# Kernel optimization log

Hardware: AMD Instinct MI355X
Metric: run time of the kernel (lower is better)

The kernel has to match this reference:

```python
import jax, jax.numpy as jnp
import numpy as np

N, D, HID, ATT, B, NC = 131072, 1024, 256, 128, 64, 2
EPS = 1e-5

def _ln(h, g, b):
    mu = jnp.mean(h, axis=-1, keepdims=True)
    var = jnp.mean((h - mu) ** 2, axis=-1, keepdims=True)
    return (h - mu) * jax.lax.rsqrt(var + EPS) * g + b

def _gelu(x):
    return jax.nn.gelu(x, approximate=False)  # torch nn.GELU default (erf)

def setup_inputs() -> dict:
    key = jax.random.key(0)
    ks = jax.random.split(key, 16)
    def w(k, shape, fan_in):
        return (jax.random.normal(k, shape, jnp.float32) / np.sqrt(fan_in)).astype(jnp.float32)
    # sorted, every bag non-empty (~equal sizes)
    segment_ids = ((jnp.arange(N) * B) // N).astype(jnp.int32)
    return {
        "x": jax.random.normal(ks[0], (N, D), jnp.float32),
        "segment_ids": segment_ids,
        "W1": w(ks[1], (D, HID), D), "b1": jnp.zeros((HID,), jnp.float32),
        "g1": jnp.ones((HID,), jnp.float32), "be1": jnp.zeros((HID,), jnp.float32),
        "W2": w(ks[2], (HID, HID), HID), "b2": jnp.zeros((HID,), jnp.float32),
        "g2": jnp.ones((HID,), jnp.float32), "be2": jnp.zeros((HID,), jnp.float32),
        "Wv": w(ks[3], (HID, ATT), HID), "bv": jnp.zeros((ATT,), jnp.float32),
        "Wu": w(ks[4], (HID, ATT), HID), "bu": jnp.zeros((ATT,), jnp.float32),
        "Ww": w(ks[5], (ATT, 1), ATT), "bw": jnp.zeros((1,), jnp.float32),
        "Wc1": w(ks[6], (HID, HID // 2), HID), "bc1": jnp.zeros((HID // 2,), jnp.float32),
        "Wc2": w(ks[7], (HID // 2, NC), HID // 2), "bc2": jnp.zeros((NC,), jnp.float32),
    }

def reference(x, segment_ids, W1, b1, g1, be1, W2, b2, g2, be2,
              Wv, bv, Wu, bu, Ww, bw, Wc1, bc1, Wc2, bc2):
    # encoder (dropout = identity at inference)
    h = _gelu(_ln(x @ W1 + b1, g1, be1))          # [N, HID]
    h = _gelu(_ln(h @ W2 + b2, g2, be2))          # [N, HID]
    # gated attention logits
    a = (jnp.tanh(h @ Wv + bv) * jax.nn.sigmoid(h @ Wu + bu)) @ Ww + bw  # [N, 1]
    a = a[:, 0]                                    # [N]
    # per-bag (segment) softmax
    m = jax.ops.segment_max(a, segment_ids, num_segments=B)             # [B]
    e = jnp.exp(a - m[segment_ids])
    s = jax.ops.segment_sum(e, segment_ids, num_segments=B)             # [B]
    attn = e / s[segment_ids]                                           # [N]
    # attention-weighted bag pooling
    z = jax.ops.segment_sum(attn[:, None] * h, segment_ids, num_segments=B)  # [B, HID]
    # classifier
    logits = _gelu(z @ Wc1 + bc1) @ Wc2 + bc2       # [B, NC]
    return logits
```

## Files before the change

kernel.cpp:

```cpp
#include <hip/hip_runtime.h>
#include <math.h>

#define N_TOK  131072
#define DIM    1024
#define HIDN   256
#define ATTN   128
#define NSEG   64
#define SEGLEN 2048
#define NCLS   2
#define EPSLN  1e-5f

typedef __attribute__((ext_vector_type(8))) short  short8;
typedef __attribute__((ext_vector_type(4))) float  f32x4;

__device__ __forceinline__ unsigned short f2bf(float f) {
    unsigned int u = __float_as_uint(f);
    u += 0x7fffu + ((u >> 16) & 1u);
    return (unsigned short)(u >> 16);
}
__device__ __forceinline__ float bf2f(unsigned short h) {
    return __uint_as_float(((unsigned int)h) << 16);
}
__device__ __forceinline__ float gelu_exact(float x) {
    return 0.5f * x * (1.0f + erff(x * 0.70710678118654752f));
}

__global__ __launch_bounds__(256) void transpose_cvt(const float* __restrict__ in,
                                                     unsigned short* __restrict__ out,
                                                     int R, int C) {
    __shared__ float t[32][33];
    const int bx = blockIdx.x * 32;
    const int by = blockIdx.y * 32;
    const int x = threadIdx.x, y = threadIdx.y;
#pragma unroll
    for (int i = 0; i < 32; i += 8) {
        int r = by + y + i, c = bx + x;
        if (r < R && c < C) t[y + i][x] = in[(size_t)r * C + c];
    }
    __syncthreads();
#pragma unroll
    for (int i = 0; i < 32; i += 8) {
        int c = bx + y + i, r = by + x;
        if (c < C && r < R) out[(size_t)c * R + r] = f2bf(t[x][y + i]);
    }
}

__global__ void build_bvu(const float* __restrict__ bv, const float* __restrict__ bu,
                          float* __restrict__ bvu) {
    int t = threadIdx.x;
    bvu[t] = (t < 128) ? bv[t] : bu[t - 128];
}

template <int K, int MODE, bool AF32>
__global__ __launch_bounds__(256, 3) void gemm_fused(const void* __restrict__ Aptr,
                                                     const unsigned short* __restrict__ Wt,
                                                     const float* __restrict__ bias,
                                                     const float* __restrict__ g,
                                                     const float* __restrict__ be,
                                                     unsigned short* __restrict__ Hout,
                                                     const float* __restrict__ Ww,
                                                     const float* __restrict__ bw,
                                                     float* __restrict__ Aout) {
    constexpr int NT = K / 32;
    __shared__ __align__(16) char smem[51200];
    auto As0 = (unsigned short (*)[40])(smem);
    auto As1 = (unsigned short (*)[40])(smem + 5120);
    auto Ws0 = (unsigned short (*)[40])(smem + 10240);
    auto Ws1 = (unsigned short (*)[40])(smem + 10240 + 20480);

    const int tid  = threadIdx.x;
    const int wave = tid >> 6, lane = tid & 63;
    const int lr = lane & 15, lq = lane >> 4;
    const int srow = tid >> 2, skq = (tid & 3) * 8;
    const size_t row0 = (size_t)blockIdx.x * 64;

    f32x4 acc[4][4];
#pragma unroll
    for (int i = 0; i < 4; i++)
#pragma unroll
        for (int j = 0; j < 4; j++) acc[i][j] = (f32x4)0.0f;

    auto loadA = [&](int k0, short8& aw) {
        if constexpr (AF32) {
            const float* A = (const float*)Aptr;
            const float* p = &A[(row0 + srow) * K + k0 + skq];
            float4 v0 = *(const float4*)p;
            float4 v1 = *(const float4*)(p + 4);
            aw[0] = (short)f2bf(v0.x); aw[1] = (short)f2bf(v0.y);
            aw[2] = (short)f2bf(v0.z); aw[3] = (short)f2bf(v0.w);
            aw[4] = (short)f2bf(v1.x); aw[5] = (short)f2bf(v1.y);
            aw[6] = (short)f2bf(v1.z); aw[7] = (short)f2bf(v1.w);
        } else {
            const unsigned short* A = (const unsigned short*)Aptr;
            aw = *(const short8*)&A[(row0 + srow) * K + k0 + skq];
        }
    };
    auto loadW = [&](int k0, short8* ww) {
#pragma unroll
        for (int c = 0; c < 4; c++)
            ww[c] = *(const short8*)&Wt[(size_t)(srow + 64 * c) * K + k0 + skq];
    };
    auto writeT = [&](unsigned short (*As)[40], unsigned short (*Ws)[40],
                      const short8& aw, const short8* ww) {
        *(short8*)&As[srow][skq] = aw;
#pragma unroll
        for (int c = 0; c < 4; c++)
            *(short8*)&Ws[srow + 64 * c][skq] = ww[c];
    };
    auto mmaT = [&](unsigned short (*As)[40], unsigned short (*Ws)[40]) {
        short8 a[4], b[4];
#pragma unroll
        for (int i = 0; i < 4; i++) a[i] = *(const short8*)&As[16 * i + lr][lq * 8];
#pragma unroll
        for (int j = 0; j < 4; j++) b[j] = *(const short8*)&Ws[64 * wave + 16 * j + lr][lq * 8];
#pragma unroll
        for (int i = 0; i < 4; i++)
#pragma unroll
            for (int j = 0; j < 4; j++)
                acc[i][j] = __builtin_amdgcn_mfma_f32_16x16x32_bf16(a[i], b[j], acc[i][j], 0, 0, 0);
    };

    short8 aw;
    short8 ww[4];
    loadA(0, aw);
    loadW(0, ww);
    writeT(As0, Ws0, aw, ww);
    __syncthreads();

    for (int t = 0; t < NT; t += 2) {
        loadA(32 * (t + 1), aw);
        loadW(32 * (t + 1), ww);
        mmaT(As0, Ws0);
        writeT(As1, Ws1, aw, ww);
        __syncthreads();
        if (t + 2 < NT) {
            loadA(32 * (t + 2), aw);
            loadW(32 * (t + 2), ww);
        }
        mmaT(As1, Ws1);
        if (t + 2 < NT) writeT(As0, Ws0, aw, ww);
        __syncthreads();
    }

    float bjv[4];
#pragma unroll
    for (int j = 0; j < 4; j++) bjv[j] = bias[wave * 64 + 16 * j + lr];
#pragma unroll
    for (int i = 0; i < 4; i++)
#pragma unroll
        for (int j = 0; j < 4; j++)
#pragma unroll
            for (int r = 0; r < 4; r++) acc[i][j][r] += bjv[j];

    if constexpr (MODE == 0) {
        float (*red)[4][64] = (float (*)[4][64])smem;
#pragma unroll
        for (int i = 0; i < 4; i++)
#pragma unroll
            for (int r = 0; r < 4; r++) {
                float s = 0.0f, sq = 0.0f;
#pragma unroll
                for (int j = 0; j < 4; j++) { float v = acc[i][j][r]; s += v; sq += v * v; }
#pragma unroll
                for (int m = 1; m < 16; m <<= 1) { s += __shfl_xor(s, m); sq += __shfl_xor(sq, m); }
                if (lr == 0) {
                    red[0][wave][16 * i + 4 * lq + r] = s;
                    red[1][wave][16 * i + 4 * lq + r] = sq;
                }
            }
        __syncthreads();
        float gj[4], bej[4];
#pragma unroll
        for (int j = 0; j < 4; j++) {
            gj[j]  = g[wave * 64 + 16 * j + lr];
            bej[j] = be[wave * 64 + 16 * j + lr];
        }
#pragma unroll
        for (int i = 0; i < 4; i++)
#pragma unroll
            for (int r = 0; r < 4; r++) {
                const int row = 16 * i + 4 * lq + r;
                const float s  = red[0][0][row] + red[0][1][row] + red[0][2][row] + red[0][3][row];
                const float sq = red[1][0][row] + red[1][1][row] + red[1][2][row] + red[1][3][row];
                const float mu  = s * (1.0f / HIDN);
                const float var = sq * (1.0f / HIDN) - mu * mu;
                const float rs  = rsqrtf(var + EPSLN);
#pragma unroll
                for (int j = 0; j < 4; j++) {
                    const float o = (acc[i][j][r] - mu) * rs * gj[j] + bej[j];
                    Hout[(row0 + row) * 256 + wave * 64 + 16 * j + lr] = f2bf(gelu_exact(o));
                }
            }
    } else {
        float (*us)[129] = (float (*)[129])smem;
        float (*pw)[64]  = (float (*)[64])(smem + 33024);
        if (wave >= 2) {
            const int cb = (wave - 2) * 64;
#pragma unroll
            for (int i = 0; i < 4; i++)
#pragma unroll
                for (int j = 0; j < 4; j++)
#pragma unroll
                    for (int r = 0; r < 4; r++)
                        us[16 * i + 4 * lq + r][cb + 16 * j + lr] =
                            1.0f / (1.0f + expf(-acc[i][j][r]));
        }
        __syncthreads();
        if (wave < 2) {
            const int cb = wave * 64;
            float wwj[4];
#pragma unroll
            for (int j = 0; j < 4; j++) wwj[j] = Ww[cb + 16 * j + lr];
#pragma unroll
            for (int i = 0; i < 4; i++)
#pragma unroll
                for (int r = 0; r < 4; r++) {
                    const int row = 16 * i + 4 * lq + r;
                    float s = 0.0f;
#pragma unroll
                    for (int j = 0; j < 4; j++)
                        s += tanhf(acc[i][j][r]) * us[row][cb + 16 * j + lr] * wwj[j];
#pragma unroll
                    for (int m = 1; m < 16; m <<= 1) s += __shfl_xor(s, m);
                    if (lr == 0) pw[wave][row] = s;
                }
        }
        __syncthreads();
        if (tid < 64) Aout[row0 + tid] = pw[0][tid] + pw[1][tid] + bw[0];
    }
}

__global__ __launch_bounds__(256) void seg_softmax(float* __restrict__ A) {
    __shared__ float red[256];
    const int seg = blockIdx.x, tid = threadIdx.x;
    float* a = A + (size_t)seg * SEGLEN;
    float m = -1e30f;
#pragma unroll
    for (int c = 0; c < 8; c++) m = fmaxf(m, a[tid + 256 * c]);
    red[tid] = m; __syncthreads();
    for (int s = 128; s > 0; s >>= 1) {
        if (tid < s) red[tid] = fmaxf(red[tid], red[tid + s]);
        __syncthreads();
    }
    m = red[0]; __syncthreads();
    float e[8]; float sum = 0.0f;
#pragma unroll
    for (int c = 0; c < 8; c++) { e[c] = expf(a[tid + 256 * c] - m); sum += e[c]; }
    red[tid] = sum; __syncthreads();
    for (int s = 128; s > 0; s >>= 1) {
        if (tid < s) red[tid] += red[tid + s];
        __syncthreads();
    }
    const float inv = 1.0f / red[0];
#pragma unroll
    for (int c = 0; c < 8; c++) a[tid + 256 * c] = e[c] * inv;
}

__global__ __launch_bounds__(256) void pool_partial(const float* __restrict__ Attn,
                                                    const unsigned short* __restrict__ H,
                                                    float* __restrict__ Zp) {
    __shared__ float aw[256];
    __shared__ float part[8][256];
    const int tid = threadIdx.x;
    const size_t rbase = (size_t)blockIdx.x * 256;
    aw[tid] = Attn[rbase + tid];
    __syncthreads();
    const int cg = tid & 31;
    const int rg = tid >> 5;
    float acc[8];
#pragma unroll
    for (int j = 0; j < 8; j++) acc[j] = 0.0f;
    for (int r = rg * 32; r < rg * 32 + 32; ++r) {
        short8 h8 = *(const short8*)&H[(rbase + r) * 256 + cg * 8];
        const float a = aw[r];
#pragma unroll
        for (int j = 0; j < 8; j++) acc[j] += a * bf2f((unsigned short)h8[j]);
    }
#pragma unroll
    for (int j = 0; j < 8; j++) part[rg][cg * 8 + j] = acc[j];
    __syncthreads();
    float s = 0.0f;
#pragma unroll
    for (int gq = 0; gq < 8; gq++) s += part[gq][tid];
    Zp[rbase + tid] = s;
}

__global__ __launch_bounds__(256) void head_kernel(const float* __restrict__ Zp,
                                                   const float* __restrict__ Wc1,
                                                   const float* __restrict__ bc1,
                                                   const float* __restrict__ Wc2,
                                                   const float* __restrict__ bc2,
                                                   float* __restrict__ Out) {
    __shared__ float zs[256];
    __shared__ float hs[128];
    __shared__ float red[4];
    const int seg = blockIdx.x, tid = threadIdx.x;
    float z = 0.0f;
#pragma unroll
    for (int c = 0; c < 8; c++) z += Zp[((size_t)seg * 8 + c) * 256 + tid];
    zs[tid] = z;
    __syncthreads();
    if (tid < 128) {
        float acc = bc1[tid];
        for (int k = 0; k < 256; k++) acc += zs[k] * Wc1[k * 128 + tid];
        hs[tid] = gelu_exact(acc);
    }
    __syncthreads();
    const int cls = tid >> 7, j = tid & 127;
    float val = hs[j] * Wc2[j * 2 + cls];
#pragma unroll
    for (int o = 32; o > 0; o >>= 1) val += __shfl_down(val, o);
    if ((tid & 63) == 0) red[tid >> 6] = val;
    __syncthreads();
    if (tid < 2) Out[seg * 2 + tid] = red[tid * 2] + red[tid * 2 + 1] + bc2[tid];
}

extern "C" void kernel_launch(void* const* d_in, const int* in_sizes, int n_in,
                              void* d_out, int out_size, void* d_ws, size_t ws_size,
                              hipStream_t stream) {
    const float* x   = (const float*)d_in[0];
    const float* W1  = (const float*)d_in[2];
    const float* b1  = (const float*)d_in[3];
    const float* g1  = (const float*)d_in[4];
    const float* be1 = (const float*)d_in[5];
    const float* W2  = (const float*)d_in[6];
    const float* b2  = (const float*)d_in[7];
    const float* g2  = (const float*)d_in[8];
    const float* be2 = (const float*)d_in[9];
    const float* Wv  = (const float*)d_in[10];
    const float* bv  = (const float*)d_in[11];
    const float* Wu  = (const float*)d_in[12];
    const float* bu  = (const float*)d_in[13];
    const float* Ww  = (const float*)d_in[14];
    const float* bw  = (const float*)d_in[15];
    const float* Wc1 = (const float*)d_in[16];
    const float* bc1 = (const float*)d_in[17];
    const float* Wc2 = (const float*)d_in[18];
    const float* bc2 = (const float*)d_in[19];
    float* out = (float*)d_out;

    char* p = (char*)d_ws;
    unsigned short* h1b    = (unsigned short*)p; p += (size_t)N_TOK * HIDN * 2;
    unsigned short* h2b    = (unsigned short*)p; p += (size_t)N_TOK * HIDN * 2;
    float*          scores = (float*)p;          p += (size_t)N_TOK * 4;
    unsigned short* W1t    = (unsigned short*)p; p += (size_t)HIDN * DIM * 2;
    unsigned short* W2t    = (unsigned short*)p; p += (size_t)HIDN * HIDN * 2;
    unsigned short* Wvut   = (unsigned short*)p; p += (size_t)HIDN * HIDN * 2;
    float*          bvu    = (float*)p;          p += 256 * 4;
    float*          Zp     = (float*)p;          p += (size_t)NSEG * 8 * HIDN * 4;

    dim3 tb(32, 8);
    transpose_cvt<<<dim3(HIDN / 32, DIM / 32), tb, 0, stream>>>(W1, W1t, DIM, HIDN);
    transpose_cvt<<<dim3(HIDN / 32, HIDN / 32), tb, 0, stream>>>(W2, W2t, HIDN, HIDN);
    transpose_cvt<<<dim3(ATTN / 32, HIDN / 32), tb, 0, stream>>>(Wv, Wvut, HIDN, ATTN);
    transpose_cvt<<<dim3(ATTN / 32, HIDN / 32), tb, 0, stream>>>(Wu, Wvut + (size_t)ATTN * HIDN, HIDN, ATTN);
    build_bvu<<<1, 256, 0, stream>>>(bv, bu, bvu);

    gemm_fused<DIM, 0, true><<<N_TOK / 64, 256, 0, stream>>>(
        x, W1t, b1, g1, be1, h1b, nullptr, nullptr, nullptr);
    gemm_fused<HIDN, 0, false><<<N_TOK / 64, 256, 0, stream>>>(
        h1b, W2t, b2, g2, be2, h2b, nullptr, nullptr, nullptr);
    gemm_fused<HIDN, 1, false><<<N_TOK / 64, 256, 0, stream>>>(
        h2b, Wvut, bvu, nullptr, nullptr, nullptr, Ww, bw, scores);

    seg_softmax<<<NSEG, 256, 0, stream>>>(scores);
    pool_partial<<<NSEG * 8, 256, 0, stream>>>(scores, h2b, Zp);
    head_kernel<<<NSEG, 256, 0, stream>>>(Zp, Wc1, bc1, Wc2, bc2, out);
}
```

Measured before the change: 1.007 ms.

## Fuse encoder MLP and attention scoring into one kernel, drop softmax pass

Merges the three per-token GEMM kernels into one kernel that keeps the first hidden layer in LDS, so the h1 round trip to global memory and the re-read of h2 for scoring are gone. Weights for the second and third GEMMs are read straight from global memory. The separate softmax kernel is removed: pool_partial exponentiates the raw scores and also writes per-block exp sums, and the head kernel divides by the segment total. The four transpose kernels and the bias-packing kernel become one launch. In exchange, the first GEMM loses its double-buffered LDS pipeline, and skipping the max subtraction relies on the gated scores staying bounded enough that exp does not overflow.

```diff
diff --git a/kernel.cpp b/kernel.cpp
--- a/kernel.cpp
+++ b/kernel.cpp
@@ -25,48 +25,51 @@
     return 0.5f * x * (1.0f + erff(x * 0.70710678118654752f));
 }
 
-__global__ __launch_bounds__(256) void transpose_cvt(const float* __restrict__ in,
-                                                     unsigned short* __restrict__ out,
-                                                     int R, int C) {
+__global__ __launch_bounds__(256) void prep_weights(const float* __restrict__ W1,
+                                                    const float* __restrict__ W2,
+                                                    const float* __restrict__ Wv,
+                                                    const float* __restrict__ Wu,
+                                                    const float* __restrict__ bv,
+                                                    const float* __restrict__ bu,
+                                                    unsigned short* __restrict__ W1t,
+                                                    unsigned short* __restrict__ W2t,
+                                                    unsigned short* __restrict__ Wvut,
+                                                    float* __restrict__ bvu) {
+    const int b = blockIdx.x;
+    const int x = threadIdx.x, y = threadIdx.y;
+    if (b == 384) {
+        const int t = y * 32 + x;
+        bvu[t] = (t < 128) ? bv[t] : bu[t - 128];
+        return;
+    }
+    const float* in; unsigned short* out; int R, C, tx, ty;
+    if (b < 256)      { in = W1; out = W1t;                        R = DIM;  C = HIDN; tx = b & 7;         ty = b >> 3; }
+    else if (b < 320) { in = W2; out = W2t;                        R = HIDN; C = HIDN; tx = (b - 256) & 7; ty = (b - 256) >> 3; }
+    else if (b < 352) { in = Wv; out = Wvut;                       R = HIDN; C = ATTN; tx = (b - 320) & 3; ty = (b - 320) >> 2; }
+    else              { in = Wu; out = Wvut + (size_t)ATTN * HIDN; R = HIDN; C = ATTN; tx = (b - 352) & 3; ty = (b - 352) >> 2; }
     __shared__ float t[32][33];
-    const int bx = blockIdx.x * 32;
-    const int by = blockIdx.y * 32;
-    const int x = threadIdx.x, y = threadIdx.y;
-#pragma unroll
-    for (int i = 0; i < 32; i += 8) {
-        int r = by + y + i, c = bx + x;
-        if (r < R && c < C) t[y + i][x] = in[(size_t)r * C + c];
-    }
-    __syncthreads();
-#pragma unroll
-    for (int i = 0; i < 32; i += 8) {
-        int c = bx + y + i, r = by + x;
-        if (c < C && r < R) out[(size_t)c * R + r] = f2bf(t[x][y + i]);
-    }
-}
-
-__global__ void build_bvu(const float* __restrict__ bv, const float* __restrict__ bu,
-                          float* __restrict__ bvu) {
-    int t = threadIdx.x;
-    bvu[t] = (t < 128) ? bv[t] : bu[t - 128];
-}
-
-template <int K, int MODE, bool AF32>
-__global__ __launch_bounds__(256, 3) void gemm_fused(const void* __restrict__ Aptr,
-                                                     const unsigned short* __restrict__ Wt,
-                                                     const float* __restrict__ bias,
-                                                     const float* __restrict__ g,
-                                                     const float* __restrict__ be,
-                                                     unsigned short* __restrict__ Hout,
-                                                     const float* __restrict__ Ww,
-                                                     const float* __restrict__ bw,
-                                                     float* __restrict__ Aout) {
-    constexpr int NT = K / 32;
-    __shared__ __align__(16) char smem[51200];
-    auto As0 = (unsigned short (*)[40])(smem);
-    auto As1 = (unsigned short (*)[40])(smem + 5120);
-    auto Ws0 = (unsigned short (*)[40])(smem + 10240);
-    auto Ws1 = (unsigned short (*)[40])(smem + 10240 + 20480);
+    const int bx = tx * 32, by = ty * 32;
+#pragma unroll
+    for (int i = 0; i < 32; i += 8) t[y + i][x] = in[(size_t)(by + y + i) * C + bx + x];
+    __syncthreads();
+#pragma unroll
+    for (int i = 0; i < 32; i += 8) out[(size_t)(bx + y + i) * R + by + x] = f2bf(t[x][y + i]);
+}
+
+__global__ __launch_bounds__(256, 3) void fused_mlp_score(
+    const float* __restrict__ x,
+    const unsigned short* __restrict__ W1t,
+    const unsigned short* __restrict__ W2t,
+    const unsigned short* __restrict__ Wvut,
+    const float* __restrict__ b1, const float* __restrict__ g1, const float* __restrict__ be1,
+    const float* __restrict__ b2, const float* __restrict__ g2, const float* __restrict__ be2,
+    const float* __restrict__ bvu, const float* __restrict__ Ww, const float* __restrict__ bw,
+    unsigned short* __restrict__ h2b, float* __restrict__ scores) {
+    __shared__ __align__(16) char smem[35840];
+    auto As  = (unsigned short (*)[40])smem;
+    auto Ws  = (unsigned short (*)[40])(smem + 5120);
+    auto HT  = (unsigned short (*)[264])smem;
+    auto red = (float (*)[4][64])(smem + 33792);
 
     const int tid  = threadIdx.x;
     const int wave = tid >> 6, lane = tid & 63;
@@ -75,85 +78,23 @@
     const size_t row0 = (size_t)blockIdx.x * 64;
 
     f32x4 acc[4][4];
-#pragma unroll
-    for (int i = 0; i < 4; i++)
-#pragma unroll
-        for (int j = 0; j < 4; j++) acc[i][j] = (f32x4)0.0f;
-
-    auto loadA = [&](int k0, short8& aw) {
-        if constexpr (AF32) {
-            const float* A = (const float*)Aptr;
-            const float* p = &A[(row0 + srow) * K + k0 + skq];
-            float4 v0 = *(const float4*)p;
-            float4 v1 = *(const float4*)(p + 4);
-            aw[0] = (short)f2bf(v0.x); aw[1] = (short)f2bf(v0.y);
-            aw[2] = (short)f2bf(v0.z); aw[3] = (short)f2bf(v0.w);
-            aw[4] = (short)f2bf(v1.x); aw[5] = (short)f2bf(v1.y);
-            aw[6] = (short)f2bf(v1.z); aw[7] = (short)f2bf(v1.w);
-        } else {
-            const unsigned short* A = (const unsigned short*)Aptr;
-            aw = *(const short8*)&A[(row0 + srow) * K + k0 + skq];
-        }
+    auto zero_acc = [&]() {
+#pragma unroll
+        for (int i = 0; i < 4; i++)
+#pragma unroll
+            for (int j = 0; j < 4; j++) acc[i][j] = (f32x4)0.0f;
     };
-    auto loadW = [&](int k0, short8* ww) {
-#pragma unroll
-        for (int c = 0; c < 4; c++)
-            ww[c] = *(const short8*)&Wt[(size_t)(srow + 64 * c) * K + k0 + skq];
-    };
-    auto writeT = [&](unsigned short (*As)[40], unsigned short (*Ws)[40],
-                      const short8& aw, const short8* ww) {
-        *(short8*)&As[srow][skq] = aw;
-#pragma unroll
-        for (int c = 0; c < 4; c++)
-            *(short8*)&Ws[srow + 64 * c][skq] = ww[c];
-    };
-    auto mmaT = [&](unsigned short (*As)[40], unsigned short (*Ws)[40]) {
-        short8 a[4], b[4];
-#pragma unroll
-        for (int i = 0; i < 4; i++) a[i] = *(const short8*)&As[16 * i + lr][lq * 8];
-#pragma unroll
-        for (int j = 0; j < 4; j++) b[j] = *(const short8*)&Ws[64 * wave + 16 * j + lr][lq * 8];
-#pragma unroll
-        for (int i = 0; i < 4; i++)
-#pragma unroll
-            for (int j = 0; j < 4; j++)
-                acc[i][j] = __builtin_amdgcn_mfma_f32_16x16x32_bf16(a[i], b[j], acc[i][j], 0, 0, 0);
-    };
-
-    short8 aw;
-    short8 ww[4];
-    loadA(0, aw);
-    loadW(0, ww);
-    writeT(As0, Ws0, aw, ww);
-    __syncthreads();
-
-    for (int t = 0; t < NT; t += 2) {
-        loadA(32 * (t + 1), aw);
-        loadW(32 * (t + 1), ww);
-        mmaT(As0, Ws0);
-        writeT(As1, Ws1, aw, ww);
-        __syncthreads();
-        if (t + 2 < NT) {
-            loadA(32 * (t + 2), aw);
-            loadW(32 * (t + 2), ww);
-        }
-        mmaT(As1, Ws1);
-        if (t + 2 < NT) writeT(As0, Ws0, aw, ww);
-        __syncthreads();
-    }
-
-    float bjv[4];
-#pragma unroll
-    for (int j = 0; j < 4; j++) bjv[j] = bias[wave * 64 + 16 * j + lr];
-#pragma unroll
-    for (int i = 0; i < 4; i++)
-#pragma unroll
-        for (int j = 0; j < 4; j++)
-#pragma unroll
-            for (int r = 0; r < 4; r++) acc[i][j][r] += bjv[j];
-
-    if constexpr (MODE == 0) {
-        float (*red)[4][64] = (float (*)[4][64])smem;
+
+    auto ln_epilogue = [&](const float* bias, const float* gamma, const float* beta, bool toGlobal) {
+        float bjv[4];
+#pragma unroll
+        for (int j = 0; j < 4; j++) bjv[j] = bias[wave * 64 + 16 * j + lr];
+#pragma unroll
+        for (int i = 0; i < 4; i++)
+#pragma unroll
+            for (int j = 0; j < 4; j++)
+#pragma unroll
+                for (int r = 0; r < 4; r++) acc[i][j][r] += bjv[j];
 #pragma unroll
         for (int i = 0; i < 4; i++)
 #pragma unroll
@@ -172,8 +113,8 @@
         float gj[4], bej[4];
 #pragma unroll
         for (int j = 0; j < 4; j++) {
-            gj[j]  = g[wave * 64 + 16 * j + lr];
-            bej[j] = be[wave * 64 + 16 * j + lr];
+            gj[j]  = gamma[wave * 64 + 16 * j + lr];
+            bej[j] = beta[wave * 64 + 16 * j + lr];
         }
 #pragma unroll
         for (int i = 0; i < 4; i++)
@@ -187,13 +128,99 @@
                 const float rs  = rsqrtf(var + EPSLN);
 #pragma unroll
                 for (int j = 0; j < 4; j++) {
-                    const float o = (acc[i][j][r] - mu) * rs * gj[j] + bej[j];
-                    Hout[(row0 + row) * 256 + wave * 64 + 16 * j + lr] = f2bf(gelu_exact(o));
+                    const int col = wave * 64 + 16 * j + lr;
+                    const unsigned short hv = f2bf(gelu_exact((acc[i][j][r] - mu) * rs * gj[j] + bej[j]));
+                    HT[row][col] = hv;
+                    if (toGlobal) h2b[(row0 + row) * 256 + col] = hv;
                 }
             }
-    } else {
+        __syncthreads();
+    };
+
+    zero_acc();
+    for (int k0 = 0; k0 < DIM; k0 += 32) {
+        const float* p = &x[(row0 + srow) * DIM + k0 + skq];
+        float4 v0 = *(const float4*)p;
+        float4 v1 = *(const float4*)(p + 4);
+        short8 aw;
+        aw[0] = (short)f2bf(v0.x); aw[1] = (short)f2bf(v0.y);
+        aw[2] = (short)f2bf(v0.z); aw[3] = (short)f2bf(v0.w);
+        aw[4] = (short)f2bf(v1.x); aw[5] = (short)f2bf(v1.y);
+        aw[6] = (short)f2bf(v1.z); aw[7] = (short)f2bf(v1.w);
+        short8 ww[4];
+#pragma unroll
+        for (int c = 0; c < 4; c++)
+            ww[c] = *(const short8*)&W1t[(size_t)(srow + 64 * c) * DIM + k0 + skq];
+        __syncthreads();
+        *(short8*)&As[srow][skq] = aw;
+#pragma unroll
+        for (int c = 0; c < 4; c++)
+            *(short8*)&Ws[srow + 64 * c][skq] = ww[c];
+        __syncthreads();
+        short8 a[4], b[4];
+#pragma unroll
+        for (int i = 0; i < 4; i++) a[i] = *(const short8*)&As[16 * i + lr][lq * 8];
+#pragma unroll
+        for (int j = 0; j < 4; j++) b[j] = *(const short8*)&Ws[64 * wave + 16 * j + lr][lq * 8];
+#pragma unroll
+        for (int i = 0; i < 4; i++)
+#pragma unroll
+            for (int j = 0; j < 4; j++)
+                acc[i][j] = __builtin_amdgcn_mfma_f32_16x16x32_bf16(a[i], b[j], acc[i][j], 0, 0, 0);
+    }
+    __syncthreads();
+    ln_epilogue(b1, g1, be1, false);
+
+    zero_acc();
+#pragma unroll 2
+    for (int t = 0; t < 8; t++) {
+        const int k0 = t * 32;
+        short8 a[4], b[4];
+#pragma unroll
+        for (int j = 0; j < 4; j++)
+            b[j] = *(const short8*)&W2t[(size_t)(64 * wave + 16 * j + lr) * HIDN + k0 + lq * 8];
+#pragma unroll
+        for (int i = 0; i < 4; i++) a[i] = *(const short8*)&HT[16 * i + lr][k0 + lq * 8];
+#pragma unroll
+        for (int i = 0; i < 4; i++)
+#pragma unroll
+            for (int j = 0; j < 4; j++)
+                acc[i][j] = __builtin_amdgcn_mfma_f32_16x16x32_bf16(a[i], b[j], acc[i][j], 0, 0, 0);
+    }
+    __syncthreads();
+    ln_epilogue(b2, g2, be2, true);
+
+    zero_acc();
+#pragma unroll 2
+    for (int t = 0; t < 8; t++) {
+        const int k0 = t * 32;
+        short8 a[4], b[4];
+#pragma unroll
+        for (int j = 0; j < 4; j++)
+            b[j] = *(const short8*)&Wvut[(size_t)(64 * wave + 16 * j + lr) * HIDN + k0 + lq * 8];
+#pragma unroll
+        for (int i = 0; i < 4; i++) a[i] = *(const short8*)&HT[16 * i + lr][k0 + lq * 8];
+#pragma unroll
+        for (int i = 0; i < 4; i++)
+#pragma unroll
+            for (int j = 0; j < 4; j++)
+                acc[i][j] = __builtin_amdgcn_mfma_f32_16x16x32_bf16(a[i], b[j], acc[i][j], 0, 0, 0);
+    }
+    __syncthreads();
+
+    {
+        float bjv[4];
+#pragma unroll
+        for (int j = 0; j < 4; j++) bjv[j] = bvu[wave * 64 + 16 * j + lr];
+#pragma unroll
+        for (int i = 0; i < 4; i++)
+#pragma unroll
+            for (int j = 0; j < 4; j++)
+#pragma unroll
+                for (int r = 0; r < 4; r++) acc[i][j][r] += bjv[j];
+
         float (*us)[129] = (float (*)[129])smem;
-        float (*pw)[64]  = (float (*)[64])(smem + 33024);
+        float (*pw)[64]  = (float (*)[64])(smem + 33792);
         if (wave >= 2) {
             const int cb = (wave - 2) * 64;
 #pragma unroll
@@ -226,44 +253,25 @@
                 }
         }
         __syncthreads();
-        if (tid < 64) Aout[row0 + tid] = pw[0][tid] + pw[1][tid] + bw[0];
-    }
-}
-
-__global__ __launch_bounds__(256) void seg_softmax(float* __restrict__ A) {
-    __shared__ float red[256];
-    const int seg = blockIdx.x, tid = threadIdx.x;
-    float* a = A + (size_t)seg * SEGLEN;
-    float m = -1e30f;
-#pragma unroll
-    for (int c = 0; c < 8; c++) m = fmaxf(m, a[tid + 256 * c]);
-    red[tid] = m; __syncthreads();
-    for (int s = 128; s > 0; s >>= 1) {
-        if (tid < s) red[tid] = fmaxf(red[tid], red[tid + s]);
-        __syncthreads();
-    }
-    m = red[0]; __syncthreads();
-    float e[8]; float sum = 0.0f;
-#pragma unroll
-    for (int c = 0; c < 8; c++) { e[c] = expf(a[tid + 256 * c] - m); sum += e[c]; }
-    red[tid] = sum; __syncthreads();
-    for (int s = 128; s > 0; s >>= 1) {
-        if (tid < s) red[tid] += red[tid + s];
-        __syncthreads();
-    }
-    const float inv = 1.0f / red[0];
-#pragma unroll
-    for (int c = 0; c < 8; c++) a[tid + 256 * c] = e[c] * inv;
-}
-
-__global__ __launch_bounds__(256) void pool_partial(const float* __restrict__ Attn,
+        if (tid < 64) scores[row0 + tid] = pw[0][tid] + pw[1][tid] + bw[0];
+    }
+}
+
+__global__ __launch_bounds__(256) void pool_partial(const float* __restrict__ Scores,
                                                     const unsigned short* __restrict__ H,
-                                                    float* __restrict__ Zp) {
+                                                    float* __restrict__ Zp,
+                                                    float* __restrict__ Se) {
     __shared__ float aw[256];
     __shared__ float part[8][256];
+    __shared__ float sred[4];
     const int tid = threadIdx.x;
     const size_t rbase = (size_t)blockIdx.x * 256;
-    aw[tid] = Attn[rbase + tid];
+    const float e = expf(Scores[rbase + tid]);
+    aw[tid] = e;
+    float se = e;
+#pragma unroll
+    for (int o = 32; o > 0; o >>= 1) se += __shfl_down(se, o);
+    if ((tid & 63) == 0) sred[tid >> 6] = se;
     __syncthreads();
     const int cg = tid & 31;
     const int rg = tid >> 5;
@@ -283,9 +291,11 @@
 #pragma unroll
     for (int gq = 0; gq < 8; gq++) s += part[gq][tid];
     Zp[rbase + tid] = s;
+    if (tid == 0) Se[blockIdx.x] = sred[0] + sred[1] + sred[2] + sred[3];
 }
 
 __global__ __launch_bounds__(256) void head_kernel(const float* __restrict__ Zp,
+                                                   const float* __restrict__ Se,
                                                    const float* __restrict__ Wc1,
                                                    const float* __restrict__ bc1,
                                                    const float* __restrict__ Wc2,
@@ -298,7 +308,10 @@
     float z = 0.0f;
 #pragma unroll
     for (int c = 0; c < 8; c++) z += Zp[((size_t)seg * 8 + c) * 256 + tid];
-    zs[tid] = z;
+    float den = 0.0f;
+#pragma unroll
+    for (int c = 0; c < 8; c++) den += Se[seg * 8 + c];
+    zs[tid] = z / den;
     __syncthreads();
     if (tid < 128) {
         float acc = bc1[tid];
@@ -340,7 +353,6 @@
     float* out = (float*)d_out;
 
     char* p = (char*)d_ws;
-    unsigned short* h1b    = (unsigned short*)p; p += (size_t)N_TOK * HIDN * 2;
     unsigned short* h2b    = (unsigned short*)p; p += (size_t)N_TOK * HIDN * 2;
     float*          scores = (float*)p;          p += (size_t)N_TOK * 4;
     unsigned short* W1t    = (unsigned short*)p; p += (size_t)HIDN * DIM * 2;
@@ -348,22 +360,15 @@
     unsigned short* Wvut   = (unsigned short*)p; p += (size_t)HIDN * HIDN * 2;
     float*          bvu    = (float*)p;          p += 256 * 4;
     float*          Zp     = (float*)p;          p += (size_t)NSEG * 8 * HIDN * 4;
-
-    dim3 tb(32, 8);
-    transpose_cvt<<<dim3(HIDN / 32, DIM / 32), tb, 0, stream>>>(W1, W1t, DIM, HIDN);
-    transpose_cvt<<<dim3(HIDN / 32, HIDN / 32), tb, 0, stream>>>(W2, W2t, HIDN, HIDN);
-    transpose_cvt<<<dim3(ATTN / 32, HIDN / 32), tb, 0, stream>>>(Wv, Wvut, HIDN, ATTN);
-    transpose_cvt<<<dim3(ATTN / 32, HIDN / 32), tb, 0, stream>>>(Wu, Wvut + (size_t)ATTN * HIDN, HIDN, ATTN);
-    build_bvu<<<1, 256, 0, stream>>>(bv, bu, bvu);
-
-    gemm_fused<DIM, 0, true><<<N_TOK / 64, 256, 0, stream>>>(
-        x, W1t, b1, g1, be1, h1b, nullptr, nullptr, nullptr);
-    gemm_fused<HIDN, 0, false><<<N_TOK / 64, 256, 0, stream>>>(
-        h1b, W2t, b2, g2, be2, h2b, nullptr, nullptr, nullptr);
-    gemm_fused<HIDN, 1, false><<<N_TOK / 64, 256, 0, stream>>>(
-        h2b, Wvut, bvu, nullptr, nullptr, nullptr, Ww, bw, scores);
-
-    seg_softmax<<<NSEG, 256, 0, stream>>>(scores);
-    pool_partial<<<NSEG * 8, 256, 0, stream>>>(scores, h2b, Zp);
-    head_kernel<<<NSEG, 256, 0, stream>>>(Zp, Wc1, bc1, Wc2, bc2, out);
-}
+    float*          Se     = (float*)p;          p += (size_t)NSEG * 8 * 4;
+
+    prep_weights<<<385, dim3(32, 8), 0, stream>>>(W1, W2, Wv, Wu, bv, bu, W1t, W2t, Wvut, bvu);
+
+    fused_mlp_score<<<N_TOK / 64, 256, 0, stream>>>(
+        x, W1t, W2t, Wvut,
+        b1, g1, be1, b2, g2, be2,
+        bvu, Ww, bw, h2b, scores);
+
+    pool_partial<<<NSEG * 8, 256, 0, stream>>>(scores, h2b, Zp, Se);
+    head_kernel<<<NSEG, 256, 0, stream>>>(Zp, Se, Wc1, bc1, Wc2, bc2, out);
+}
```

Result: slower. 1.343 ms (+33.3%).
